# Kernel optimization log

Hardware: AMD Instinct MI355X
Metric: run time of the kernel (lower is better)

Reference implementation:

```python
import jax, jax.numpy as jnp
import numpy as np

B, N, C, H, E = 16, 512, 128, 8, 131072
Nn = B * N
Dh = C // H
EPS = 1e-5


def setup_inputs() -> dict:
    key = jax.random.key(0)
    ks = jax.random.split(key, 16)
    s = C ** -0.5
    x = jax.random.normal(ks[0], (Nn, C), dtype=jnp.float32)
    edge_index = jax.random.randint(ks[1], (2, E), 0, Nn)
    batch = jnp.arange(Nn) // N  # B equal-sized graphs, sorted
    attn_bias = jax.random.normal(ks[2], (B, N, N, H), dtype=jnp.float32)
    return {
        "x": x,
        "edge_index": edge_index,
        "batch": batch,
        "attn_bias": attn_bias,
        "conv_w": jax.random.normal(ks[3], (C, C)) * s,
        "conv_b": jnp.zeros((C,)),
        "wq": jax.random.normal(ks[4], (C, C)) * s,
        "bq": jnp.zeros((C,)),
        "wk": jax.random.normal(ks[5], (C, C)) * s,
        "bk": jnp.zeros((C,)),
        "wv": jax.random.normal(ks[6], (C, C)) * s,
        "bv": jnp.zeros((C,)),
        "wo": jax.random.normal(ks[7], (C, C)) * s,
        "bo": jnp.zeros((C,)),
        "w1": jax.random.normal(ks[8], (C, 2 * C)) * s,
        "b1": jnp.zeros((2 * C,)),
        "w2": jax.random.normal(ks[9], (2 * C, C)) * (2 * C) ** -0.5,
        "b2": jnp.zeros((C,)),
        "g1": jnp.ones((C,)), "be1": jnp.zeros((C,)),
        "g2": jnp.ones((C,)), "be2": jnp.zeros((C,)),
        "g3": jnp.ones((C,)), "be3": jnp.zeros((C,)),
    }


def _bn(h, g, b):
    # BatchNorm1d over the node dimension (training-mode batch statistics)
    mu = h.mean(axis=0)
    var = h.var(axis=0)  # biased, matches torch normalization
    return g * (h - mu) * jax.lax.rsqrt(var + EPS) + b


def reference(x, edge_index, batch, attn_bias,
              conv_w, conv_b, wq, bq, wk, bk, wv, bv, wo, bo,
              w1, b1, w2, b2, g1, be1, g2, be2, g3, be3):
    n_nodes, ch = x.shape
    bsz, n_max, _, heads = attn_bias.shape
    dh = ch // heads

    # ---- GCN conv (self loops + symmetric norm) -> dropout(0) + residual + norm1
    loops = jnp.arange(n_nodes)
    src = jnp.concatenate([edge_index[0], loops])
    dst = jnp.concatenate([edge_index[1], loops])
    deg = jax.ops.segment_sum(jnp.ones_like(src, dtype=x.dtype), dst, num_segments=n_nodes)
    dinv = jax.lax.rsqrt(jnp.maximum(deg, 1.0))
    xw = x @ conv_w
    msg = xw[src] * (dinv[src] * dinv[dst])[:, None]
    hconv = jax.ops.segment_sum(msg, dst, num_segments=n_nodes) + conv_b
    h1 = _bn(hconv + x, g1, be1)

    # ---- dense batch (equal-sized sorted graphs -> pure reshape, mask all-valid)
    xd = x.reshape(bsz, n_max, ch)
    q = ((xd @ wq + bq) * (dh ** -0.5)).reshape(bsz, n_max, heads, dh)
    k = (xd @ wk + bk).reshape(bsz, n_max, heads, dh)
    v = (xd @ wv + bv).reshape(bsz, n_max, heads, dh)
    scores = jnp.einsum('bqhd,bkhd->bqkh', q, k) + attn_bias  # [B,N,N,H]
    probs = jax.nn.softmax(scores, axis=2)
    att = jnp.einsum('bqkh,bkhd->bqhd', probs, v).reshape(bsz, n_max, ch)
    att = att @ wo + bo
    h2 = _bn(att.reshape(n_nodes, ch) + x, g2, be2)

    # ---- combine branches, MLP with residual, norm3
    out = h1 + h2
    mlp = jax.nn.relu(out @ w1 + b1) @ w2 + b2
    return _bn(out + mlp, g3, be3)
```

## Files before the change

kernel.cpp:

```cpp
#include <hip/hip_runtime.h>
#include <cstddef>

#define NN 8192
#define CC 128

typedef unsigned short u16;
typedef _Float16 half_t;
typedef _Float16 v4h __attribute__((ext_vector_type(4)));
typedef float v4f __attribute__((ext_vector_type(4)));

typedef __attribute__((address_space(3))) void lvoid_t;
static __device__ inline unsigned lds_addr(void* p) {
  return (unsigned)(unsigned long long)(lvoid_t*)p;
}


__global__ __launch_bounds__(256) void count_deg_int_k(const int* __restrict__ dst, int* degi, int E) {
  int i = blockIdx.x * 256 + threadIdx.x;
  if (i < E) atomicAdd(&degi[dst[i]], 1);
}

__global__ __launch_bounds__(256) void dinv_k(const int* __restrict__ degi, float* __restrict__ dinv, int n) {
  int i = blockIdx.x * 256 + threadIdx.x;
  if (i < n) dinv[i] = rsqrtf((float)(degi[i] + 1));
}

__global__ __launch_bounds__(256) void scan_k(const int* __restrict__ degi, int* __restrict__ rowstart,
                                              int* __restrict__ cursor) {
  __shared__ int partial[256];
  int t = threadIdx.x;
  int base = t * 32;
  int local[32];
  int s = 0;
#pragma unroll
  for (int i = 0; i < 32; ++i) { local[i] = s; s += degi[base + i]; }
  partial[t] = s;
  __syncthreads();
  for (int off = 1; off < 256; off <<= 1) {
    int v = (t >= off) ? partial[t - off] : 0;
    __syncthreads();
    partial[t] += v;
    __syncthreads();
  }
  int offset = partial[t] - s;
#pragma unroll
  for (int i = 0; i < 32; ++i) {
    rowstart[base + i] = offset + local[i];
    cursor[base + i] = offset + local[i];
  }
  if (t == 255) rowstart[NN] = offset + s;
}

__global__ __launch_bounds__(256) void bucket_k(const int* __restrict__ src, const int* __restrict__ dst,
    int* __restrict__ cursor, int* __restrict__ col, int E) {
  int e = blockIdx.x * 256 + threadIdx.x;
  if (e >= E) return;
  int d = dst[e];
  int pos = atomicAdd(&cursor[d], 1);
  col[pos] = src[e];
}

__global__ __launch_bounds__(256) void gather_k(const int* __restrict__ rowstart, const int* __restrict__ col,
    const float* __restrict__ xws, const float* __restrict__ dinv, const float* __restrict__ cb,
    const float* __restrict__ x, float* __restrict__ h1) {
  int d = blockIdx.x * 2 + (threadIdx.x >> 7);
  int c = threadIdx.x & 127;
  int j0 = rowstart[d], j1 = rowstart[d + 1];
  float dd = dinv[d];
  float sum = 0.f;
  float v = 0.f;
  if (j0 < j1) v = xws[(size_t)col[j0] * CC + c];
  for (int j = j0; j < j1; ++j) {
    float v_next = 0.f;
    if (j + 1 < j1) v_next = xws[(size_t)col[j + 1] * CC + c];
    sum += v;
    v = v_next;
  }
  int idx = d * CC + c;
  sum += xws[idx];
  h1[idx] = sum * dd + cb[c] + x[idx];
}


__global__ __launch_bounds__(256) void bn_stats_k(const float* __restrict__ X,
    float* __restrict__ sums, float* __restrict__ sumsq) {
  int t = threadIdx.x;
  int c = t & 127, rg = t >> 7;
  int r0 = blockIdx.x * 64;
  float s = 0.f, sq = 0.f;
  for (int i = 0; i < 32; ++i) {
    float v = X[(size_t)(r0 + rg + 2 * i) * CC + c];
    s += v; sq += v * v;
  }
  atomicAdd(&sums[c], s);
  atomicAdd(&sumsq[c], sq);
}

__global__ __launch_bounds__(256) void combine_k(const float* __restrict__ h1, const float* __restrict__ h2,
    const float* __restrict__ st, const float* __restrict__ g1, const float* __restrict__ be1,
    const float* __restrict__ g2, const float* __restrict__ be2, float* __restrict__ out) {
  int idx = blockIdx.x * 256 + threadIdx.x;
  int c = idx & 127;
  float mu1 = st[c] * (1.f / NN);
  float var1 = st[128 + c] * (1.f / NN) - mu1 * mu1;
  float sc1 = g1[c] * rsqrtf(var1 + 1e-5f);
  float sh1 = be1[c] - mu1 * sc1;
  float mu2 = st[256 + c] * (1.f / NN);
  float var2 = st[384 + c] * (1.f / NN) - mu2 * mu2;
  float sc2 = g2[c] * rsqrtf(var2 + 1e-5f);
  float sh2 = be2[c] - mu2 * sc2;
  out[idx] = sc1 * h1[idx] + sh1 + sc2 * h2[idx] + sh2;
}

__global__ __launch_bounds__(256) void bn_apply_k(const float* __restrict__ h, const float* __restrict__ st,
    const float* __restrict__ g3, const float* __restrict__ be3, float* __restrict__ out) {
  int idx = blockIdx.x * 256 + threadIdx.x;
  int c = idx & 127;
  float mu = st[512 + c] * (1.f / NN);
  float var = st[640 + c] * (1.f / NN) - mu * mu;
  float sc = g3[c] * rsqrtf(var + 1e-5f);
  float sh = be3[c] - mu * sc;
  out[idx] = sc * h[idx] + sh;
}

__global__ __launch_bounds__(256) void gemm_k(const float* __restrict__ A, const float* __restrict__ W,
    const float* __restrict__ bias, const float* __restrict__ resid, const float* __restrict__ dscale,
    float* __restrict__ out, int M, int N, int K, float scale, int relu, int ofp16) {
  __shared__ float As[64 * 132];
  __shared__ float Ws[128 * 64];
  int t = threadIdx.x;
  int ty = t >> 4, tx = t & 15;
  int row0 = blockIdx.x * 64, n0 = blockIdx.y * 64;
  float acc[4][4] = {};
  for (int kc = 0; kc < K; kc += 128) {
#pragma unroll
    for (int j = 0; j < 8; ++j) {
      int f = t + 256 * j;
      int r = f >> 5, c4 = f & 31;
      *(float4*)(As + r * 132 + c4 * 4) = *(const float4*)(A + (size_t)(row0 + r) * K + kc + c4 * 4);
    }
#pragma unroll
    for (int j = 0; j < 8; ++j) {
      int f = t + 256 * j;
      int kr = f >> 4, c4 = f & 15;
      *(float4*)(Ws + kr * 64 + c4 * 4) = *(const float4*)(W + (size_t)(kc + kr) * N + n0 + c4 * 4);
    }
    __syncthreads();
    for (int k0 = 0; k0 < 128; k0 += 4) {
      float a[4][4], b[4][4];
#pragma unroll
      for (int i = 0; i < 4; ++i) {
        float4 t4 = *(const float4*)(As + (4 * ty + i) * 132 + k0);
        a[i][0] = t4.x; a[i][1] = t4.y; a[i][2] = t4.z; a[i][3] = t4.w;
      }
#pragma unroll
      for (int kk = 0; kk < 4; ++kk) {
        float4 t4 = *(const float4*)(Ws + (k0 + kk) * 64 + 4 * tx);
        b[kk][0] = t4.x; b[kk][1] = t4.y; b[kk][2] = t4.z; b[kk][3] = t4.w;
      }
#pragma unroll
      for (int kk = 0; kk < 4; ++kk)
#pragma unroll
        for (int i = 0; i < 4; ++i)
#pragma unroll
          for (int j = 0; j < 4; ++j)
            acc[i][j] += a[i][kk] * b[kk][j];
    }
    __syncthreads();
  }
  float4 bv = make_float4(0.f, 0.f, 0.f, 0.f);
  if (bias) bv = *(const float4*)(bias + n0 + 4 * tx);
#pragma unroll
  for (int i = 0; i < 4; ++i) {
    int row = row0 + 4 * ty + i;
    float ds = dscale ? dscale[row] : 1.f;
    float4 r;
    r.x = (acc[i][0] + bv.x) * scale * ds;
    r.y = (acc[i][1] + bv.y) * scale * ds;
    r.z = (acc[i][2] + bv.z) * scale * ds;
    r.w = (acc[i][3] + bv.w) * scale * ds;
    if (relu) { r.x = fmaxf(r.x, 0.f); r.y = fmaxf(r.y, 0.f); r.z = fmaxf(r.z, 0.f); r.w = fmaxf(r.w, 0.f); }
    size_t o = (size_t)row * N + n0 + 4 * tx;
    if (ofp16) {
      half_t* oh = (half_t*)out;
      v4h hv;
      hv[0] = (half_t)r.x; hv[1] = (half_t)r.y; hv[2] = (half_t)r.z; hv[3] = (half_t)r.w;
      *(v4h*)(oh + o) = hv;
    } else {
      if (resid) {
        float4 rv = *(const float4*)(resid + o);
        r.x += rv.x; r.y += rv.y; r.z += rv.z; r.w += rv.w;
      }
      *(float4*)(out + o) = r;
    }
  }
}

__global__ __launch_bounds__(256, 2) void attn_k(const half_t* __restrict__ Qh,
    const half_t* __restrict__ Kh, const half_t* __restrict__ Vh, const float* __restrict__ bias,
    float* __restrict__ out) {
  __shared__ u16 VL[4][2][2048];
  __shared__ float LB[4][8][16];
  const int t = threadIdx.x;
  const int wv = t >> 6;
  const int l = t & 63;
  const int qtg = blockIdx.x;
  const int b = qtg >> 5;
  const int node_t = qtg * 16;
  const int key0 = wv * 128;
  const int kb0 = b * 512 + key0;
  const int lq = l & 15;
  const int lg = l >> 4;

  v4h qf[8];
#pragma unroll
  for (int hd = 0; hd < 8; ++hd)
    qf[hd] = *(const v4h*)(Qh + (size_t)(node_t + lq) * CC + hd * 16 + lg * 4);

  v4f oacc[8];
  float lacc[8];
#pragma unroll
  for (int hd = 0; hd < 8; ++hd) { oacc[hd] = (v4f){0.f, 0.f, 0.f, 0.f}; lacc[hd] = 0.f; }

  const int v_hdb = l >> 5;
  const int v_kg = (l >> 3) & 3;
  const int v_km = (l >> 1) & 3;
  const int v_dm0 = (l & 1) * 8;
  uint4 vreg[4];

  auto vload = [&](int ch) {
#pragma unroll
    for (int i = 0; i < 4; ++i)
      vreg[i] = *(const uint4*)(Vh + (size_t)(kb0 + ch * 16 + v_kg * 4 + v_km) * CC
                                + (i * 2 + v_hdb) * 16 + v_dm0);
  };
  auto vwrite = [&](int bf) {
#pragma unroll
    for (int i = 0; i < 4; ++i)
      *(uint4*)&VL[wv][bf][i * 512 + l * 8] = vreg[i];
  };

  const unsigned lbase = lds_addr(&VL[wv][0][0]);
  const float* bb = bias + ((size_t)node_t * 512 + key0) * 8 + (size_t)lq * 4096;

  vload(0);
  vwrite(0);

  for (int ch = 0; ch < 8; ++ch) {
    const int bf = ch & 1;
    if (ch < 7) vload(ch + 1);

    v4h kf[8];
#pragma unroll
    for (int hd = 0; hd < 8; ++hd)
      kf[hd] = *(const v4h*)(Kh + (size_t)(kb0 + ch * 16 + lq) * CC + hd * 16 + lg * 4);

    asm volatile("s_waitcnt lgkmcnt(0)" ::: "memory");
    __builtin_amdgcn_sched_barrier(0);
    unsigned va = lbase + (unsigned)(bf * 4096) + (unsigned)(l * 8);
    unsigned long long vfr[8];
#pragma unroll
    for (int hd = 0; hd < 8; ++hd)
      asm volatile("ds_read_b64_tr_b16 %0, %1 offset:%2"
                   : "=v"(vfr[hd]) : "v"(va), "i"(hd * 512));
    asm volatile("s_waitcnt lgkmcnt(0)" ::: "memory");
    __builtin_amdgcn_sched_barrier(0);

    if (ch < 7) vwrite(bf ^ 1);

    const v4f z = (v4f){0.f, 0.f, 0.f, 0.f};
#pragma unroll
    for (int hg = 0; hg < 2; ++hg) {
      v4f bfr[4];
#pragma unroll
      for (int reg = 0; reg < 4; ++reg)
        bfr[reg] = *(const v4f*)(bb + (size_t)(ch * 16 + lg * 4 + reg) * 8 + hg * 4);

      v4f stv[4];
#pragma unroll
      for (int j = 0; j < 4; ++j)
        stv[j] = __builtin_amdgcn_mfma_f32_16x16x16f16(kf[hg * 4 + j], qf[hg * 4 + j], z, 0, 0, 0);

#pragma unroll
      for (int j = 0; j < 4; ++j) {
        const int hd = hg * 4 + j;
        float pr0 = __expf(stv[j][0] + bfr[0][j] - 4.f);
        float pr1 = __expf(stv[j][1] + bfr[1][j] - 4.f);
        float pr2 = __expf(stv[j][2] + bfr[2][j] - 4.f);
        float pr3 = __expf(stv[j][3] + bfr[3][j] - 4.f);
        lacc[hd] += pr0 + pr1 + pr2 + pr3;
        unsigned u0 = __builtin_bit_cast(unsigned, __builtin_amdgcn_cvt_pkrtz(pr0, pr1));
        unsigned u1 = __builtin_bit_cast(unsigned, __builtin_amdgcn_cvt_pkrtz(pr2, pr3));
        uint2 pu = make_uint2(u0, u1);
        v4h pa = __builtin_bit_cast(v4h, pu);
        v4h vf = __builtin_bit_cast(v4h, vfr[hd]);
        oacc[hd] = __builtin_amdgcn_mfma_f32_16x16x16f16(pa, vf, oacc[hd], 0, 0, 0);
      }
    }
  }

#pragma unroll
  for (int hd = 0; hd < 8; ++hd) {
    float v = lacc[hd];
    v += __shfl_xor(v, 16);
    v += __shfl_xor(v, 32);
    lacc[hd] = v;
  }
  if (l < 16) {
#pragma unroll
    for (int hd = 0; hd < 8; ++hd)
      LB[wv][hd][l] = lacc[hd];
  }

  float* FB = (float*)VL;
#pragma unroll
  for (int hd = 0; hd < 8; ++hd)
#pragma unroll
    for (int reg = 0; reg < 4; ++reg)
      FB[wv * 2048 + (lg * 4 + reg) * 128 + hd * 16 + lq] = oacc[hd][reg];

  __syncthreads();

  const int q = t >> 4, d0 = (t & 15) * 8;
  float res[8];
#pragma unroll
  for (int j = 0; j < 8; ++j) {
    int d = d0 + j, hd = d >> 4;
    float v = FB[q * 128 + d] + FB[2048 + q * 128 + d]
            + FB[4096 + q * 128 + d] + FB[6144 + q * 128 + d];
    float L = LB[0][hd][q] + LB[1][hd][q] + LB[2][hd][q] + LB[3][hd][q];
    res[j] = v / L;
  }
  float* po = out + (size_t)(node_t + q) * CC + d0;
  *(float4*)po       = make_float4(res[0], res[1], res[2], res[3]);
  *(float4*)(po + 4) = make_float4(res[4], res[5], res[6], res[7]);
}


extern "C" void kernel_launch(void* const* d_in, const int* in_sizes, int n_in,
                              void* d_out, int out_size, void* d_ws, size_t ws_size,
                              hipStream_t stream) {
  const float* x      = (const float*)d_in[0];
  const int*   ei     = (const int*)d_in[1];
  const float* bias   = (const float*)d_in[3];
  const float* conv_w = (const float*)d_in[4];
  const float* conv_b = (const float*)d_in[5];
  const float* wq = (const float*)d_in[6];
  const float* bq = (const float*)d_in[7];
  const float* wk = (const float*)d_in[8];
  const float* bk = (const float*)d_in[9];
  const float* wv = (const float*)d_in[10];
  const float* bv = (const float*)d_in[11];
  const float* wo = (const float*)d_in[12];
  const float* bo = (const float*)d_in[13];
  const float* w1 = (const float*)d_in[14];
  const float* b1 = (const float*)d_in[15];
  const float* w2 = (const float*)d_in[16];
  const float* b2 = (const float*)d_in[17];
  const float* g1 = (const float*)d_in[18];
  const float* be1 = (const float*)d_in[19];
  const float* g2 = (const float*)d_in[20];
  const float* be2 = (const float*)d_in[21];
  const float* g3 = (const float*)d_in[22];
  const float* be3 = (const float*)d_in[23];
  int E = in_sizes[1] / 2;

  float* ws = (float*)d_ws;
  const size_t NC = (size_t)NN * CC;
  float* xw     = ws;
  float* h1pre  = ws + NC;
  float* qb     = ws + 2 * NC;
  float* kb     = ws + 3 * NC;
  float* vb     = ws + 4 * NC;
  float* h2pre  = ws + 5 * NC;
  float* outbuf = ws + 6 * NC;
  float* hid    = ws + 2 * NC;
  float* h3pre  = ws + 4 * NC;
  float* st     = ws + 7 * NC;
  float* dinv   = ws + 7 * NC + 768;
  int*   degi     = (int*)(ws + 7 * NC + 768 + NN);
  int*   rowstart = degi + NN;
  int*   cursor   = rowstart + NN + 1;
  int*   col      = cursor + NN;

  hipMemsetAsync(degi, 0, NN * sizeof(int), stream);
  hipMemsetAsync(st, 0, 768 * sizeof(float), stream);

  count_deg_int_k<<<(E + 255) / 256, 256, 0, stream>>>(ei + E, degi, E);
  dinv_k<<<NN / 256, 256, 0, stream>>>(degi, dinv, NN);
  scan_k<<<1, 256, 0, stream>>>(degi, rowstart, cursor);
  bucket_k<<<(E + 255) / 256, 256, 0, stream>>>(ei, ei + E, cursor, col, E);
  gemm_k<<<dim3(NN / 64, 2), 256, 0, stream>>>(x, conv_w, nullptr, nullptr, dinv, xw, NN, CC, CC, 1.f, 0, 0);
  gather_k<<<NN / 2, 256, 0, stream>>>(rowstart, col, xw, dinv, conv_b, x, h1pre);
  bn_stats_k<<<NN / 64, 256, 0, stream>>>(h1pre, st + 0, st + 128);

  gemm_k<<<dim3(NN / 64, 2), 256, 0, stream>>>(x, wq, bq, nullptr, nullptr, qb, NN, CC, CC, 0.25f, 0, 1);
  gemm_k<<<dim3(NN / 64, 2), 256, 0, stream>>>(x, wk, bk, nullptr, nullptr, kb, NN, CC, CC, 1.f, 0, 1);
  gemm_k<<<dim3(NN / 64, 2), 256, 0, stream>>>(x, wv, bv, nullptr, nullptr, vb, NN, CC, CC, 1.f, 0, 1);
  attn_k<<<512, 256, 0, stream>>>((const half_t*)qb, (const half_t*)kb, (const half_t*)vb, bias, outbuf);
  gemm_k<<<dim3(NN / 64, 2), 256, 0, stream>>>(outbuf, wo, bo, x, nullptr, h2pre, NN, CC, CC, 1.f, 0, 0);
  bn_stats_k<<<NN / 64, 256, 0, stream>>>(h2pre, st + 256, st + 384);

  combine_k<<<NC / 256, 256, 0, stream>>>(h1pre, h2pre, st, g1, be1, g2, be2, outbuf);
  gemm_k<<<dim3(NN / 64, 4), 256, 0, stream>>>(outbuf, w1, b1, nullptr, nullptr, hid, NN, 2 * CC, CC, 1.f, 1, 0);
  gemm_k<<<dim3(NN / 64, 2), 256, 0, stream>>>(hid, w2, b2, outbuf, nullptr, h3pre, NN, CC, 2 * CC, 1.f, 0, 0);
  bn_stats_k<<<NN / 64, 256, 0, stream>>>(h3pre, st + 512, st + 640);
  bn_apply_k<<<NC / 256, 256, 0, stream>>>(h3pre, st, g3, be3, (float*)d_out);
}
```

Before: 413.9 us.

## Replace FP32 SIMT GEMMs with FP16 MFMA GEMM and fold dinv into scan

Swaps the scalar FP32 tiled GEMM for a templated MFMA 16x16x16 f16 kernel. Each block handles 16 rows by 128 columns, stages the weights as f16 in LDS and reads them with transposing LDS loads, with a double-buffered read pipeline. This is meant to cut the compute cost of the seven dense projection GEMMs. It also removes a separate launch by computing dinv inside the scan kernel. Inputs are rounded to fp16 for the matmuls, which lowers precision and changes the accuracy of the FP32 outputs, and each block reloads the full weight slice.

Measured after the change: 409.7 us. Within noise of the previous version (-1.0%).

```diff
diff --git a/kernel.cpp b/kernel.cpp
--- a/kernel.cpp
+++ b/kernel.cpp
@@ -20,20 +20,19 @@
   if (i < E) atomicAdd(&degi[dst[i]], 1);
 }
 
-__global__ __launch_bounds__(256) void dinv_k(const int* __restrict__ degi, float* __restrict__ dinv, int n) {
-  int i = blockIdx.x * 256 + threadIdx.x;
-  if (i < n) dinv[i] = rsqrtf((float)(degi[i] + 1));
-}
-
 __global__ __launch_bounds__(256) void scan_k(const int* __restrict__ degi, int* __restrict__ rowstart,
-                                              int* __restrict__ cursor) {
+                                              int* __restrict__ cursor, float* __restrict__ dinv) {
   __shared__ int partial[256];
   int t = threadIdx.x;
   int base = t * 32;
   int local[32];
   int s = 0;
 #pragma unroll
-  for (int i = 0; i < 32; ++i) { local[i] = s; s += degi[base + i]; }
+  for (int i = 0; i < 32; ++i) {
+    int d = degi[base + i];
+    dinv[base + i] = rsqrtf((float)(d + 1));
+    local[i] = s; s += d;
+  }
   partial[t] = s;
   __syncthreads();
   for (int off = 1; off < 256; off <<= 1) {
@@ -123,75 +122,91 @@
   out[idx] = sc * h[idx] + sh;
 }
 
-__global__ __launch_bounds__(256) void gemm_k(const float* __restrict__ A, const float* __restrict__ W,
+template <int KT>
+__global__ __launch_bounds__(256, 2) void mgemm_k(const float* __restrict__ A, const float* __restrict__ W,
     const float* __restrict__ bias, const float* __restrict__ resid, const float* __restrict__ dscale,
-    float* __restrict__ out, int M, int N, int K, float scale, int relu, int ofp16) {
-  __shared__ float As[64 * 132];
-  __shared__ float Ws[128 * 64];
-  int t = threadIdx.x;
-  int ty = t >> 4, tx = t & 15;
-  int row0 = blockIdx.x * 64, n0 = blockIdx.y * 64;
-  float acc[4][4] = {};
-  for (int kc = 0; kc < K; kc += 128) {
-#pragma unroll
-    for (int j = 0; j < 8; ++j) {
-      int f = t + 256 * j;
-      int r = f >> 5, c4 = f & 31;
-      *(float4*)(As + r * 132 + c4 * 4) = *(const float4*)(A + (size_t)(row0 + r) * K + kc + c4 * 4);
+    float* __restrict__ out, int N, float scale, int relu, int ofp16) {
+  constexpr int NCH = KT / 16;
+  __shared__ u16 WL[NCH][2048];
+  const int t = threadIdx.x;
+  const int wv = t >> 6, l = t & 63;
+  const int row0 = blockIdx.x * 16;
+  const int n0 = blockIdx.y * 128;
+  const int lq = l & 15, lg = l >> 4;
+
+  const int s_hdb = l >> 5;
+  const int s_kg = (l >> 3) & 3;
+  const int s_km = (l >> 1) & 3;
+  const int s_dm0 = (l & 1) * 8;
+  for (int ch = wv; ch < NCH; ch += 4) {
+    int krow = ch * 16 + s_kg * 4 + s_km;
+    const float* wr = W + (size_t)krow * N + n0;
+#pragma unroll
+    for (int i = 0; i < 4; ++i) {
+      const float* src = wr + (i * 2 + s_hdb) * 16 + s_dm0;
+      float4 f0 = *(const float4*)src;
+      float4 f1 = *(const float4*)(src + 4);
+      unsigned u0 = __builtin_bit_cast(unsigned, __builtin_amdgcn_cvt_pkrtz(f0.x, f0.y));
+      unsigned u1 = __builtin_bit_cast(unsigned, __builtin_amdgcn_cvt_pkrtz(f0.z, f0.w));
+      unsigned u2 = __builtin_bit_cast(unsigned, __builtin_amdgcn_cvt_pkrtz(f1.x, f1.y));
+      unsigned u3 = __builtin_bit_cast(unsigned, __builtin_amdgcn_cvt_pkrtz(f1.z, f1.w));
+      *(uint4*)&WL[ch][i * 512 + l * 8] = make_uint4(u0, u1, u2, u3);
     }
-#pragma unroll
-    for (int j = 0; j < 8; ++j) {
-      int f = t + 256 * j;
-      int kr = f >> 4, c4 = f & 15;
-      *(float4*)(Ws + kr * 64 + c4 * 4) = *(const float4*)(W + (size_t)(kc + kr) * N + n0 + c4 * 4);
+  }
+
+  v4f af[NCH];
+#pragma unroll
+  for (int i = 0; i < NCH; ++i)
+    af[i] = *(const v4f*)(A + (size_t)(row0 + lq) * KT + i * 16 + lg * 4);
+
+  __syncthreads();
+
+  v4f acc[2];
+  acc[0] = (v4f){0.f, 0.f, 0.f, 0.f};
+  acc[1] = (v4f){0.f, 0.f, 0.f, 0.f};
+  const unsigned va0 = lds_addr(&WL[0][0]) + (unsigned)(wv * 1024 + l * 8);
+
+  unsigned long long cur0, cur1, nxt0, nxt1;
+  asm volatile("ds_read_b64_tr_b16 %0, %2 offset:0\n\t"
+               "ds_read_b64_tr_b16 %1, %2 offset:512"
+               : "=v"(cur0), "=v"(cur1) : "v"(va0));
+#pragma unroll
+  for (int i = 0; i < NCH; ++i) {
+    if (i + 1 < NCH) {
+      unsigned va = va0 + (unsigned)((i + 1) * 4096);
+      asm volatile("ds_read_b64_tr_b16 %0, %2 offset:0\n\t"
+                   "ds_read_b64_tr_b16 %1, %2 offset:512"
+                   : "=v"(nxt0), "=v"(nxt1) : "v"(va));
+      asm volatile("s_waitcnt lgkmcnt(2)" ::: "memory");
+    } else {
+      asm volatile("s_waitcnt lgkmcnt(0)" ::: "memory");
     }
-    __syncthreads();
-    for (int k0 = 0; k0 < 128; k0 += 4) {
-      float a[4][4], b[4][4];
-#pragma unroll
-      for (int i = 0; i < 4; ++i) {
-        float4 t4 = *(const float4*)(As + (4 * ty + i) * 132 + k0);
-        a[i][0] = t4.x; a[i][1] = t4.y; a[i][2] = t4.z; a[i][3] = t4.w;
+    __builtin_amdgcn_sched_barrier(0);
+    v4h a;
+    a[0] = (half_t)af[i][0]; a[1] = (half_t)af[i][1];
+    a[2] = (half_t)af[i][2]; a[3] = (half_t)af[i][3];
+    acc[0] = __builtin_amdgcn_mfma_f32_16x16x16f16(a, __builtin_bit_cast(v4h, cur0), acc[0], 0, 0, 0);
+    acc[1] = __builtin_amdgcn_mfma_f32_16x16x16f16(a, __builtin_bit_cast(v4h, cur1), acc[1], 0, 0, 0);
+    cur0 = nxt0; cur1 = nxt1;
+  }
+
+#pragma unroll
+  for (int c = 0; c < 2; ++c) {
+    int hd = wv * 2 + c;
+    float bcv = bias ? bias[n0 + hd * 16 + lq] : 0.f;
+#pragma unroll
+    for (int reg = 0; reg < 4; ++reg) {
+      int row = row0 + lg * 4 + reg;
+      float ds = dscale ? dscale[row] : 1.f;
+      float r = (acc[c][reg] + bcv) * scale * ds;
+      if (relu) r = fmaxf(r, 0.f);
+      size_t o = (size_t)row * N + n0 + hd * 16 + lq;
+      if (ofp16) {
+        ((half_t*)out)[o] = (half_t)r;
+      } else {
+        if (resid) r += resid[o];
+        out[o] = r;
       }
-#pragma unroll
-      for (int kk = 0; kk < 4; ++kk) {
-        float4 t4 = *(const float4*)(Ws + (k0 + kk) * 64 + 4 * tx);
-        b[kk][0] = t4.x; b[kk][1] = t4.y; b[kk][2] = t4.z; b[kk][3] = t4.w;
-      }
-#pragma unroll
-      for (int kk = 0; kk < 4; ++kk)
-#pragma unroll
-        for (int i = 0; i < 4; ++i)
-#pragma unroll
-          for (int j = 0; j < 4; ++j)
-            acc[i][j] += a[i][kk] * b[kk][j];
-    }
-    __syncthreads();
-  }
-  float4 bv = make_float4(0.f, 0.f, 0.f, 0.f);
-  if (bias) bv = *(const float4*)(bias + n0 + 4 * tx);
-#pragma unroll
-  for (int i = 0; i < 4; ++i) {
-    int row = row0 + 4 * ty + i;
-    float ds = dscale ? dscale[row] : 1.f;
-    float4 r;
-    r.x = (acc[i][0] + bv.x) * scale * ds;
-    r.y = (acc[i][1] + bv.y) * scale * ds;
-    r.z = (acc[i][2] + bv.z) * scale * ds;
-    r.w = (acc[i][3] + bv.w) * scale * ds;
-    if (relu) { r.x = fmaxf(r.x, 0.f); r.y = fmaxf(r.y, 0.f); r.z = fmaxf(r.z, 0.f); r.w = fmaxf(r.w, 0.f); }
-    size_t o = (size_t)row * N + n0 + 4 * tx;
-    if (ofp16) {
-      half_t* oh = (half_t*)out;
-      v4h hv;
-      hv[0] = (half_t)r.x; hv[1] = (half_t)r.y; hv[2] = (half_t)r.z; hv[3] = (half_t)r.w;
-      *(v4h*)(oh + o) = hv;
-    } else {
-      if (resid) {
-        float4 rv = *(const float4*)(resid + o);
-        r.x += rv.x; r.y += rv.y; r.z += rv.z; r.w += rv.w;
-      }
-      *(float4*)(out + o) = r;
     }
   }
 }
@@ -387,23 +402,22 @@
   hipMemsetAsync(st, 0, 768 * sizeof(float), stream);
 
   count_deg_int_k<<<(E + 255) / 256, 256, 0, stream>>>(ei + E, degi, E);
-  dinv_k<<<NN / 256, 256, 0, stream>>>(degi, dinv, NN);
-  scan_k<<<1, 256, 0, stream>>>(degi, rowstart, cursor);
+  scan_k<<<1, 256, 0, stream>>>(degi, rowstart, cursor, dinv);
   bucket_k<<<(E + 255) / 256, 256, 0, stream>>>(ei, ei + E, cursor, col, E);
-  gemm_k<<<dim3(NN / 64, 2), 256, 0, stream>>>(x, conv_w, nullptr, nullptr, dinv, xw, NN, CC, CC, 1.f, 0, 0);
+  mgemm_k<128><<<dim3(NN / 16, 1), 256, 0, stream>>>(x, conv_w, nullptr, nullptr, dinv, xw, CC, 1.f, 0, 0);
   gather_k<<<NN / 2, 256, 0, stream>>>(rowstart, col, xw, dinv, conv_b, x, h1pre);
   bn_stats_k<<<NN / 64, 256, 0, stream>>>(h1pre, st + 0, st + 128);
 
-  gemm_k<<<dim3(NN / 64, 2), 256, 0, stream>>>(x, wq, bq, nullptr, nullptr, qb, NN, CC, CC, 0.25f, 0, 1);
-  gemm_k<<<dim3(NN / 64, 2), 256, 0, stream>>>(x, wk, bk, nullptr, nullptr, kb, NN, CC, CC, 1.f, 0, 1);
-  gemm_k<<<dim3(NN / 64, 2), 256, 0, stream>>>(x, wv, bv, nullptr, nullptr, vb, NN, CC, CC, 1.f, 0, 1);
+  mgemm_k<128><<<dim3(NN / 16, 1), 256, 0, stream>>>(x, wq, bq, nullptr, nullptr, qb, CC, 0.25f, 0, 1);
+  mgemm_k<128><<<dim3(NN / 16, 1), 256, 0, stream>>>(x, wk, bk, nullptr, nullptr, kb, CC, 1.f, 0, 1);
+  mgemm_k<128><<<dim3(NN / 16, 1), 256, 0, stream>>>(x, wv, bv, nullptr, nullptr, vb, CC, 1.f, 0, 1);
   attn_k<<<512, 256, 0, stream>>>((const half_t*)qb, (const half_t*)kb, (const half_t*)vb, bias, outbuf);
-  gemm_k<<<dim3(NN / 64, 2), 256, 0, stream>>>(outbuf, wo, bo, x, nullptr, h2pre, NN, CC, CC, 1.f, 0, 0);
+  mgemm_k<128><<<dim3(NN / 16, 1), 256, 0, stream>>>(outbuf, wo, bo, x, nullptr, h2pre, CC, 1.f, 0, 0);
   bn_stats_k<<<NN / 64, 256, 0, stream>>>(h2pre, st + 256, st + 384);
 
   combine_k<<<NC / 256, 256, 0, stream>>>(h1pre, h2pre, st, g1, be1, g2, be2, outbuf);
-  gemm_k<<<dim3(NN / 64, 4), 256, 0, stream>>>(outbuf, w1, b1, nullptr, nullptr, hid, NN, 2 * CC, CC, 1.f, 1, 0);
-  gemm_k<<<dim3(NN / 64, 2), 256, 0, stream>>>(hid, w2, b2, outbuf, nullptr, h3pre, NN, CC, 2 * CC, 1.f, 0, 0);
+  mgemm_k<128><<<dim3(NN / 16, 2), 256, 0, stream>>>(outbuf, w1, b1, nullptr, nullptr, hid, 2 * CC, 1.f, 1, 0);
+  mgemm_k<256><<<dim3(NN / 16, 1), 256, 0, stream>>>(hid, w2, b2, outbuf, nullptr, h3pre, CC, 1.f, 0, 0);
   bn_stats_k<<<NN / 64, 256, 0, stream>>>(h3pre, st + 512, st + 640);
   bn_apply_k<<<NC / 256, 256, 0, stream>>>(h3pre, st, g3, be3, (float*)d_out);
 }
```
